# Performance work log

Hardware: AMD Instinct MI355X
Metric: run time of the kernel (lower is better)

## Reference

```python
import jax, jax.numpy as jnp
import numpy as np

N, E, H, DK = 50000, 800000, 8, 32


def setup_inputs() -> dict:
    key = jax.random.key(0)
    ks = jax.random.split(key, 5)
    q = jax.random.normal(ks[0], (N, H, DK), dtype=jnp.float32)
    k = jax.random.normal(ks[1], (N, H, DK), dtype=jnp.float32)
    v = jax.random.normal(ks[2], (N, H, DK), dtype=jnp.float32)
    src = jax.random.randint(ks[3], (E,), 0, N)
    dst = jax.random.randint(ks[4], (E,), 0, N)
    return {"q": q, "k": k, "v": v, "src": src, "dst": dst}


def reference(q, k, v, src, dst):
    # src_dot_dst('k','q','score'): per-edge, per-head dot product  [E, H]
    score = jnp.sum(k[src] * q[dst], axis=-1)
    # scaled_exp('score', sqrt(d_k)): exp(clamp(score/sqrt(d_k), -5, 5))
    inv_scale = 1.0 / jnp.sqrt(jnp.asarray(q.shape[-1], q.dtype))
    score = jnp.exp(jnp.clip(score * inv_scale, -5.0, 5.0))
    n = q.shape[0]
    # send_and_recv(src_mul_edge('v','score'), sum) -> wv[dst] += v[src]*score
    wv = jax.ops.segment_sum(v[src] * score[..., None], dst, num_segments=n)
    # send_and_recv(copy_edge('score'), sum) -> z[dst] += score
    z = jax.ops.segment_sum(score, dst, num_segments=n)
    return wv, z
```

## Files before the change

kernel.cpp:

```cpp
#include <hip/hip_runtime.h>
#include <math.h>

#define HEADS 8
#define DKDIM 32
#define REC   (HEADS * DKDIM)

__device__ __forceinline__ unsigned short f2bf_rne(float f) {
    unsigned int u = __float_as_uint(f);
    unsigned int r = u + 0x7fffu + ((u >> 16) & 1u);
    return (unsigned short)(r >> 16);
}
__device__ __forceinline__ float lo16(unsigned int u) { return __uint_as_float(u << 16); }
__device__ __forceinline__ float hi16(unsigned int u) { return __uint_as_float(u & 0xffff0000u); }

__global__ __launch_bounds__(256) void prep_kernel(
    const float* __restrict__ k, const float* __restrict__ v,
    uint4* __restrict__ kvb, int total_chunks,
    const int* __restrict__ dst, int* __restrict__ hist, int E)
{
    const int stride = gridDim.x * blockDim.x;
    for (int i = blockIdx.x * blockDim.x + threadIdx.x; i < total_chunks; i += stride) {
        const float4 kf = ((const float4*)k)[i];
        const float4 vf = ((const float4*)v)[i];
        uint4 o;
        o.x = (unsigned)f2bf_rne(kf.x) | ((unsigned)f2bf_rne(kf.y) << 16);
        o.y = (unsigned)f2bf_rne(kf.z) | ((unsigned)f2bf_rne(kf.w) << 16);
        o.z = (unsigned)f2bf_rne(vf.x) | ((unsigned)f2bf_rne(vf.y) << 16);
        o.w = (unsigned)f2bf_rne(vf.z) | ((unsigned)f2bf_rne(vf.w) << 16);
        kvb[i] = o;
    }
    for (int i = blockIdx.x * blockDim.x + threadIdx.x; i < E; i += stride) {
        atomicAdd(&hist[dst[i]], 1);
    }
}

__global__ __launch_bounds__(256) void scan_part_kernel(const int* __restrict__ hist,
                                                        int* __restrict__ bsum, int n) {
    const int t = threadIdx.x, lane = t & 63, wid = t >> 6;
    const int i = blockIdx.x * 256 + t;
    int x = (i < n) ? hist[i] : 0;
    #pragma unroll
    for (int off = 1; off < 64; off <<= 1) x += __shfl_xor(x, off, 64);
    __shared__ int ws[4];
    if (lane == 0) ws[wid] = x;
    __syncthreads();
    if (t == 0) bsum[blockIdx.x] = ws[0] + ws[1] + ws[2] + ws[3];
}

__global__ __launch_bounds__(256) void scan_block_kernel(int* __restrict__ bsum, int nb) {
    const int t = threadIdx.x, lane = t & 63, wid = t >> 6;
    int x = (t < nb) ? bsum[t] : 0;
    int inc = x;
    #pragma unroll
    for (int off = 1; off < 64; off <<= 1) {
        int y = __shfl_up(inc, off, 64);
        if (lane >= off) inc += y;
    }
    __shared__ int ws[4];
    if (lane == 63) ws[wid] = inc;
    __syncthreads();
    int base = 0;
    for (int w = 0; w < wid; ++w) base += ws[w];
    if (t < nb) bsum[t] = base + inc - x;
}

__global__ __launch_bounds__(256) void scan_fix_kernel(const int* __restrict__ hist,
                                                       const int* __restrict__ bsum,
                                                       int* __restrict__ rowptr, int n) {
    const int t = threadIdx.x, lane = t & 63, wid = t >> 6;
    const int i = blockIdx.x * 256 + t;
    int x = (i < n) ? hist[i] : 0;
    int inc = x;
    #pragma unroll
    for (int off = 1; off < 64; off <<= 1) {
        int y = __shfl_up(inc, off, 64);
        if (lane >= off) inc += y;
    }
    __shared__ int ws[4];
    if (lane == 63) ws[wid] = inc;
    __syncthreads();
    int base = bsum[blockIdx.x];
    for (int w = 0; w < wid; ++w) base += ws[w];
    if (i < n) rowptr[i] = base + inc - x;
}

__global__ void scatter_kernel(const int* __restrict__ src, const int* __restrict__ dst,
                               int* __restrict__ rowptr,
                               int* __restrict__ sorted_src, int E) {
    int i = blockIdx.x * blockDim.x + threadIdx.x;
    const int stride = gridDim.x * blockDim.x;
    for (; i < E; i += stride) {
        const int pos = atomicAdd(&rowptr[dst[i]], 1);
        sorted_src[pos] = src[i];
    }
}

__global__ __launch_bounds__(256) void node_kernel_bf16(
    const float* __restrict__ q, const uint4* __restrict__ kvb,
    const int* __restrict__ rowptr, const int* __restrict__ hist,
    const int* __restrict__ sorted_src,
    float* __restrict__ wv, float* __restrict__ z, int nodes)
{
    const int lane = threadIdx.x & 63;
    const int node = blockIdx.x * 4 + (threadIdx.x >> 6);
    if (node >= nodes) return;
    const int h = lane >> 3;
    const float inv_scale = 0.17677669529663687f;

    const float4 qf = ((const float4*)(q + (size_t)node * REC))[lane];
    float4 acc = {0.f, 0.f, 0.f, 0.f};
    float zacc = 0.f;

    const int end = rowptr[node];
    const int beg = end - hist[node];
    int i = beg;
    for (; i + 3 < end; i += 4) {
        const int s0 = sorted_src[i];
        const int s1 = sorted_src[i + 1];
        const int s2 = sorted_src[i + 2];
        const int s3 = sorted_src[i + 3];
        const uint4 c0 = kvb[(size_t)s0 * 64 + lane];
        const uint4 c1 = kvb[(size_t)s1 * 64 + lane];
        const uint4 c2 = kvb[(size_t)s2 * 64 + lane];
        const uint4 c3 = kvb[(size_t)s3 * 64 + lane];

        float p0 = lo16(c0.x) * qf.x + hi16(c0.x) * qf.y + lo16(c0.y) * qf.z + hi16(c0.y) * qf.w;
        float p1 = lo16(c1.x) * qf.x + hi16(c1.x) * qf.y + lo16(c1.y) * qf.z + hi16(c1.y) * qf.w;
        float p2 = lo16(c2.x) * qf.x + hi16(c2.x) * qf.y + lo16(c2.y) * qf.z + hi16(c2.y) * qf.w;
        float p3 = lo16(c3.x) * qf.x + hi16(c3.x) * qf.y + lo16(c3.y) * qf.z + hi16(c3.y) * qf.w;
        p0 += __shfl_xor(p0, 4, 8); p1 += __shfl_xor(p1, 4, 8);
        p2 += __shfl_xor(p2, 4, 8); p3 += __shfl_xor(p3, 4, 8);
        p0 += __shfl_xor(p0, 2, 8); p1 += __shfl_xor(p1, 2, 8);
        p2 += __shfl_xor(p2, 2, 8); p3 += __shfl_xor(p3, 2, 8);
        p0 += __shfl_xor(p0, 1, 8); p1 += __shfl_xor(p1, 1, 8);
        p2 += __shfl_xor(p2, 1, 8); p3 += __shfl_xor(p3, 1, 8);
        const float sc0 = __expf(fminf(fmaxf(p0 * inv_scale, -5.0f), 5.0f));
        const float sc1 = __expf(fminf(fmaxf(p1 * inv_scale, -5.0f), 5.0f));
        const float sc2 = __expf(fminf(fmaxf(p2 * inv_scale, -5.0f), 5.0f));
        const float sc3 = __expf(fminf(fmaxf(p3 * inv_scale, -5.0f), 5.0f));

        acc.x += lo16(c0.z) * sc0 + lo16(c1.z) * sc1 + lo16(c2.z) * sc2 + lo16(c3.z) * sc3;
        acc.y += hi16(c0.z) * sc0 + hi16(c1.z) * sc1 + hi16(c2.z) * sc2 + hi16(c3.z) * sc3;
        acc.z += lo16(c0.w) * sc0 + lo16(c1.w) * sc1 + lo16(c2.w) * sc2 + lo16(c3.w) * sc3;
        acc.w += hi16(c0.w) * sc0 + hi16(c1.w) * sc1 + hi16(c2.w) * sc2 + hi16(c3.w) * sc3;
        zacc += (sc0 + sc1) + (sc2 + sc3);
    }
    for (; i < end; ++i) {
        const int s0 = sorted_src[i];
        const uint4 c0 = kvb[(size_t)s0 * 64 + lane];
        float p0 = lo16(c0.x) * qf.x + hi16(c0.x) * qf.y + lo16(c0.y) * qf.z + hi16(c0.y) * qf.w;
        p0 += __shfl_xor(p0, 4, 8);
        p0 += __shfl_xor(p0, 2, 8);
        p0 += __shfl_xor(p0, 1, 8);
        const float sc0 = __expf(fminf(fmaxf(p0 * inv_scale, -5.0f), 5.0f));
        acc.x += lo16(c0.z) * sc0;
        acc.y += hi16(c0.z) * sc0;
        acc.z += lo16(c0.w) * sc0;
        acc.w += hi16(c0.w) * sc0;
        zacc += sc0;
    }
    ((float4*)(wv + (size_t)node * REC))[lane] = acc;
    if ((lane & 7) == 0) z[(size_t)node * HEADS + h] = zacc;
}

__global__ __launch_bounds__(256) void node_kernel_f32(
    const float* __restrict__ q, const float* __restrict__ k,
    const float* __restrict__ v,
    const int* __restrict__ rowptr, const int* __restrict__ hist,
    const int* __restrict__ sorted_src,
    float* __restrict__ wv, float* __restrict__ z, int nodes)
{
    const int lane = threadIdx.x & 63;
    const int node = blockIdx.x * 4 + (threadIdx.x >> 6);
    if (node >= nodes) return;
    const int h = lane >> 3;
    const float inv_scale = 0.17677669529663687f;

    const float4 qf = ((const float4*)(q + (size_t)node * REC))[lane];
    float4 acc = {0.f, 0.f, 0.f, 0.f};
    float zacc = 0.f;

    const int end = rowptr[node];
    const int beg = end - hist[node];
    for (int i = beg; i < end; ++i) {
        const int s = sorted_src[i];
        const float4 kf = ((const float4*)(k + (size_t)s * REC))[lane];
        float p = kf.x * qf.x + kf.y * qf.y + kf.z * qf.z + kf.w * qf.w;
        p += __shfl_xor(p, 4, 8);
        p += __shfl_xor(p, 2, 8);
        p += __shfl_xor(p, 1, 8);
        const float score = __expf(fminf(fmaxf(p * inv_scale, -5.0f), 5.0f));
        const float4 vf = ((const float4*)(v + (size_t)s * REC))[lane];
        acc.x += vf.x * score;
        acc.y += vf.y * score;
        acc.z += vf.z * score;
        acc.w += vf.w * score;
        zacc += score;
    }
    ((float4*)(wv + (size_t)node * REC))[lane] = acc;
    if ((lane & 7) == 0) z[(size_t)node * HEADS + h] = zacc;
}

extern "C" void kernel_launch(void* const* d_in, const int* in_sizes, int n_in,
                              void* d_out, int out_size, void* d_ws, size_t ws_size,
                              hipStream_t stream) {
    const float* q  = (const float*)d_in[0];
    const float* k  = (const float*)d_in[1];
    const float* v  = (const float*)d_in[2];
    const int* src  = (const int*)d_in[3];
    const int* dst  = (const int*)d_in[4];
    const int E     = in_sizes[3];
    const int nodes = in_sizes[0] / REC;

    float* wv = (float*)d_out;
    float* z  = wv + (size_t)nodes * REC;

    const int nb = (nodes + 255) / 256;
    const size_t kv_bytes  = (size_t)nodes * 64 * sizeof(uint4);
    const size_t int_count = (size_t)2 * nodes + nb + (size_t)E;
    const bool use_bf16 = ws_size >= kv_bytes + int_count * sizeof(int);

    char* wsb = (char*)d_ws;
    uint4* kvb = (uint4*)wsb;
    int* ints  = use_bf16 ? (int*)(wsb + kv_bytes) : (int*)wsb;
    int* hist       = ints;
    int* rowptr     = hist + nodes;
    int* bsum       = rowptr + nodes;
    int* sorted_src = bsum + nb;

    hipMemsetAsync(hist, 0, (size_t)nodes * sizeof(int), stream);
    if (use_bf16) {
        prep_kernel<<<2048, 256, 0, stream>>>(k, v, kvb, nodes * 64, dst, hist, E);
    } else {
        prep_kernel<<<2048, 256, 0, stream>>>(k, v, kvb, 0, dst, hist, E);
    }
    scan_part_kernel<<<nb, 256, 0, stream>>>(hist, bsum, nodes);
    scan_block_kernel<<<1, 256, 0, stream>>>(bsum, nb);
    scan_fix_kernel<<<nb, 256, 0, stream>>>(hist, bsum, rowptr, nodes);
    scatter_kernel<<<1024, 256, 0, stream>>>(src, dst, rowptr, sorted_src, E);
    if (use_bf16)
        node_kernel_bf16<<<(nodes + 3) / 4, 256, 0, stream>>>(q, kvb, rowptr, hist,
                                                              sorted_src, wv, z, nodes);
    else
        node_kernel_f32<<<(nodes + 3) / 4, 256, 0, stream>>>(q, k, v, rowptr, hist,
                                                             sorted_src, wv, z, nodes);
}
```

Measured before the change: 240.0 us.

## Move bf16 conversion into scatter kernel, use rowptr neighbors, unroll by two

Moves the k/v bf16 packing out of the histogram kernel and into the scatter kernel, leaving a small standalone hist kernel with its own grid size. The node kernels now take segment bounds from adjacent post-scatter rowptr entries instead of reading hist, and make the node index wave-uniform with readfirstlane. The bf16 edge loop is unrolled by two instead of four, which uses fewer registers but keeps fewer gathers in flight. The intent is to rebalance work across the pre-processing kernels and to cut per-node loads and register pressure in the gather kernel.

```diff
diff --git a/kernel.cpp b/kernel.cpp
--- a/kernel.cpp
+++ b/kernel.cpp
@@ -13,25 +13,12 @@
 __device__ __forceinline__ float lo16(unsigned int u) { return __uint_as_float(u << 16); }
 __device__ __forceinline__ float hi16(unsigned int u) { return __uint_as_float(u & 0xffff0000u); }
 
-__global__ __launch_bounds__(256) void prep_kernel(
-    const float* __restrict__ k, const float* __restrict__ v,
-    uint4* __restrict__ kvb, int total_chunks,
+__global__ __launch_bounds__(256) void hist_kernel(
     const int* __restrict__ dst, int* __restrict__ hist, int E)
 {
+    int i = blockIdx.x * blockDim.x + threadIdx.x;
     const int stride = gridDim.x * blockDim.x;
-    for (int i = blockIdx.x * blockDim.x + threadIdx.x; i < total_chunks; i += stride) {
-        const float4 kf = ((const float4*)k)[i];
-        const float4 vf = ((const float4*)v)[i];
-        uint4 o;
-        o.x = (unsigned)f2bf_rne(kf.x) | ((unsigned)f2bf_rne(kf.y) << 16);
-        o.y = (unsigned)f2bf_rne(kf.z) | ((unsigned)f2bf_rne(kf.w) << 16);
-        o.z = (unsigned)f2bf_rne(vf.x) | ((unsigned)f2bf_rne(vf.y) << 16);
-        o.w = (unsigned)f2bf_rne(vf.z) | ((unsigned)f2bf_rne(vf.w) << 16);
-        kvb[i] = o;
-    }
-    for (int i = blockIdx.x * blockDim.x + threadIdx.x; i < E; i += stride) {
-        atomicAdd(&hist[dst[i]], 1);
-    }
+    for (; i < E; i += stride) atomicAdd(&hist[dst[i]], 1);
 }
 
 __global__ __launch_bounds__(256) void scan_part_kernel(const int* __restrict__ hist,
@@ -84,26 +71,38 @@
     if (i < n) rowptr[i] = base + inc - x;
 }
 
-__global__ void scatter_kernel(const int* __restrict__ src, const int* __restrict__ dst,
-                               int* __restrict__ rowptr,
-                               int* __restrict__ sorted_src, int E) {
-    int i = blockIdx.x * blockDim.x + threadIdx.x;
+__global__ __launch_bounds__(256) void scatter_convert_kernel(
+    const int* __restrict__ src, const int* __restrict__ dst,
+    int* __restrict__ rowptr, int* __restrict__ sorted_src, int E,
+    const float* __restrict__ k, const float* __restrict__ v,
+    uint4* __restrict__ kvb, int total_chunks)
+{
     const int stride = gridDim.x * blockDim.x;
-    for (; i < E; i += stride) {
+    for (int i = blockIdx.x * blockDim.x + threadIdx.x; i < E; i += stride) {
         const int pos = atomicAdd(&rowptr[dst[i]], 1);
         sorted_src[pos] = src[i];
     }
+    for (int i = blockIdx.x * blockDim.x + threadIdx.x; i < total_chunks; i += stride) {
+        const float4 kf = ((const float4*)k)[i];
+        const float4 vf = ((const float4*)v)[i];
+        uint4 o;
+        o.x = (unsigned)f2bf_rne(kf.x) | ((unsigned)f2bf_rne(kf.y) << 16);
+        o.y = (unsigned)f2bf_rne(kf.z) | ((unsigned)f2bf_rne(kf.w) << 16);
+        o.z = (unsigned)f2bf_rne(vf.x) | ((unsigned)f2bf_rne(vf.y) << 16);
+        o.w = (unsigned)f2bf_rne(vf.z) | ((unsigned)f2bf_rne(vf.w) << 16);
+        kvb[i] = o;
+    }
 }
 
 __global__ __launch_bounds__(256) void node_kernel_bf16(
     const float* __restrict__ q, const uint4* __restrict__ kvb,
-    const int* __restrict__ rowptr, const int* __restrict__ hist,
-    const int* __restrict__ sorted_src,
+    const int* __restrict__ rowptr, const int* __restrict__ sorted_src,
     float* __restrict__ wv, float* __restrict__ z, int nodes)
 {
     const int lane = threadIdx.x & 63;
-    const int node = blockIdx.x * 4 + (threadIdx.x >> 6);
+    int node = blockIdx.x * 4 + (threadIdx.x >> 6);
     if (node >= nodes) return;
+    node = __builtin_amdgcn_readfirstlane(node);
     const int h = lane >> 3;
     const float inv_scale = 0.17677669529663687f;
 
@@ -111,44 +110,36 @@
     float4 acc = {0.f, 0.f, 0.f, 0.f};
     float zacc = 0.f;
 
+    const int beg = (node > 0) ? rowptr[node - 1] : 0;
     const int end = rowptr[node];
-    const int beg = end - hist[node];
     int i = beg;
-    for (; i + 3 < end; i += 4) {
+    for (; i + 1 < end; i += 2) {
         const int s0 = sorted_src[i];
         const int s1 = sorted_src[i + 1];
-        const int s2 = sorted_src[i + 2];
-        const int s3 = sorted_src[i + 3];
         const uint4 c0 = kvb[(size_t)s0 * 64 + lane];
         const uint4 c1 = kvb[(size_t)s1 * 64 + lane];
-        const uint4 c2 = kvb[(size_t)s2 * 64 + lane];
-        const uint4 c3 = kvb[(size_t)s3 * 64 + lane];
-
-        float p0 = lo16(c0.x) * qf.x + hi16(c0.x) * qf.y + lo16(c0.y) * qf.z + hi16(c0.y) * qf.w;
-        float p1 = lo16(c1.x) * qf.x + hi16(c1.x) * qf.y + lo16(c1.y) * qf.z + hi16(c1.y) * qf.w;
-        float p2 = lo16(c2.x) * qf.x + hi16(c2.x) * qf.y + lo16(c2.y) * qf.z + hi16(c2.y) * qf.w;
-        float p3 = lo16(c3.x) * qf.x + hi16(c3.x) * qf.y + lo16(c3.y) * qf.z + hi16(c3.y) * qf.w;
+
+        float p0 = lo16(c0.x) * qf.x + hi16(c0.x) * qf.y
+                 + lo16(c0.y) * qf.z + hi16(c0.y) * qf.w;
+        float p1 = lo16(c1.x) * qf.x + hi16(c1.x) * qf.y
+                 + lo16(c1.y) * qf.z + hi16(c1.y) * qf.w;
         p0 += __shfl_xor(p0, 4, 8); p1 += __shfl_xor(p1, 4, 8);
-        p2 += __shfl_xor(p2, 4, 8); p3 += __shfl_xor(p3, 4, 8);
         p0 += __shfl_xor(p0, 2, 8); p1 += __shfl_xor(p1, 2, 8);
-        p2 += __shfl_xor(p2, 2, 8); p3 += __shfl_xor(p3, 2, 8);
         p0 += __shfl_xor(p0, 1, 8); p1 += __shfl_xor(p1, 1, 8);
-        p2 += __shfl_xor(p2, 1, 8); p3 += __shfl_xor(p3, 1, 8);
         const float sc0 = __expf(fminf(fmaxf(p0 * inv_scale, -5.0f), 5.0f));
         const float sc1 = __expf(fminf(fmaxf(p1 * inv_scale, -5.0f), 5.0f));
-        const float sc2 = __expf(fminf(fmaxf(p2 * inv_scale, -5.0f), 5.0f));
-        const float sc3 = __expf(fminf(fmaxf(p3 * inv_scale, -5.0f), 5.0f));
-
-        acc.x += lo16(c0.z) * sc0 + lo16(c1.z) * sc1 + lo16(c2.z) * sc2 + lo16(c3.z) * sc3;
-        acc.y += hi16(c0.z) * sc0 + hi16(c1.z) * sc1 + hi16(c2.z) * sc2 + hi16(c3.z) * sc3;
-        acc.z += lo16(c0.w) * sc0 + lo16(c1.w) * sc1 + lo16(c2.w) * sc2 + lo16(c3.w) * sc3;
-        acc.w += hi16(c0.w) * sc0 + hi16(c1.w) * sc1 + hi16(c2.w) * sc2 + hi16(c3.w) * sc3;
-        zacc += (sc0 + sc1) + (sc2 + sc3);
-    }
-    for (; i < end; ++i) {
+
+        acc.x += lo16(c0.z) * sc0 + lo16(c1.z) * sc1;
+        acc.y += hi16(c0.z) * sc0 + hi16(c1.z) * sc1;
+        acc.z += lo16(c0.w) * sc0 + lo16(c1.w) * sc1;
+        acc.w += hi16(c0.w) * sc0 + hi16(c1.w) * sc1;
+        zacc += sc0 + sc1;
+    }
+    if (i < end) {
         const int s0 = sorted_src[i];
         const uint4 c0 = kvb[(size_t)s0 * 64 + lane];
-        float p0 = lo16(c0.x) * qf.x + hi16(c0.x) * qf.y + lo16(c0.y) * qf.z + hi16(c0.y) * qf.w;
+        float p0 = lo16(c0.x) * qf.x + hi16(c0.x) * qf.y
+                 + lo16(c0.y) * qf.z + hi16(c0.y) * qf.w;
         p0 += __shfl_xor(p0, 4, 8);
         p0 += __shfl_xor(p0, 2, 8);
         p0 += __shfl_xor(p0, 1, 8);
@@ -166,13 +157,13 @@
 __global__ __launch_bounds__(256) void node_kernel_f32(
     const float* __restrict__ q, const float* __restrict__ k,
     const float* __restrict__ v,
-    const int* __restrict__ rowptr, const int* __restrict__ hist,
-    const int* __restrict__ sorted_src,
+    const int* __restrict__ rowptr, const int* __restrict__ sorted_src,
     float* __restrict__ wv, float* __restrict__ z, int nodes)
 {
     const int lane = threadIdx.x & 63;
-    const int node = blockIdx.x * 4 + (threadIdx.x >> 6);
+    int node = blockIdx.x * 4 + (threadIdx.x >> 6);
     if (node >= nodes) return;
+    node = __builtin_amdgcn_readfirstlane(node);
     const int h = lane >> 3;
     const float inv_scale = 0.17677669529663687f;
 
@@ -180,8 +171,8 @@
     float4 acc = {0.f, 0.f, 0.f, 0.f};
     float zacc = 0.f;
 
+    const int beg = (node > 0) ? rowptr[node - 1] : 0;
     const int end = rowptr[node];
-    const int beg = end - hist[node];
     for (int i = beg; i < end; ++i) {
         const int s = sorted_src[i];
         const float4 kf = ((const float4*)(k + (size_t)s * REC))[lane];
@@ -215,9 +206,9 @@
     float* wv = (float*)d_out;
     float* z  = wv + (size_t)nodes * REC;
 
-    const int nb = (nodes + 255) / 256;
+    const int nbp = (nodes + 255) / 256;
     const size_t kv_bytes  = (size_t)nodes * 64 * sizeof(uint4);
-    const size_t int_count = (size_t)2 * nodes + nb + (size_t)E;
+    const size_t int_count = (size_t)2 * nodes + nbp + (size_t)E;
     const bool use_bf16 = ws_size >= kv_bytes + int_count * sizeof(int);
 
     char* wsb = (char*)d_ws;
@@ -226,22 +217,19 @@
     int* hist       = ints;
     int* rowptr     = hist + nodes;
     int* bsum       = rowptr + nodes;
-    int* sorted_src = bsum + nb;
+    int* sorted_src = bsum + nbp;
 
     hipMemsetAsync(hist, 0, (size_t)nodes * sizeof(int), stream);
-    if (use_bf16) {
-        prep_kernel<<<2048, 256, 0, stream>>>(k, v, kvb, nodes * 64, dst, hist, E);
-    } else {
-        prep_kernel<<<2048, 256, 0, stream>>>(k, v, kvb, 0, dst, hist, E);
-    }
-    scan_part_kernel<<<nb, 256, 0, stream>>>(hist, bsum, nodes);
-    scan_block_kernel<<<1, 256, 0, stream>>>(bsum, nb);
-    scan_fix_kernel<<<nb, 256, 0, stream>>>(hist, bsum, rowptr, nodes);
-    scatter_kernel<<<1024, 256, 0, stream>>>(src, dst, rowptr, sorted_src, E);
+    hist_kernel<<<800, 256, 0, stream>>>(dst, hist, E);
+    scan_part_kernel<<<nbp, 256, 0, stream>>>(hist, bsum, nodes);
+    scan_block_kernel<<<1, 256, 0, stream>>>(bsum, nbp);
+    scan_fix_kernel<<<nbp, 256, 0, stream>>>(hist, bsum, rowptr, nodes);
+    scatter_convert_kernel<<<2048, 256, 0, stream>>>(
+        src, dst, rowptr, sorted_src, E, k, v, kvb, use_bf16 ? nodes * 64 : 0);
     if (use_bf16)
-        node_kernel_bf16<<<(nodes + 3) / 4, 256, 0, stream>>>(q, kvb, rowptr, hist,
-                                                              sorted_src, wv, z, nodes);
+        node_kernel_bf16<<<(nodes + 3) / 4, 256, 0, stream>>>(
+            q, kvb, rowptr, sorted_src, wv, z, nodes);
     else
-        node_kernel_f32<<<(nodes + 3) / 4, 256, 0, stream>>>(q, k, v, rowptr, hist,
-                                                             sorted_src, wv, z, nodes);
-}
+        node_kernel_f32<<<(nodes + 3) / 4, 256, 0, stream>>>(
+            q, k, v, rowptr, sorted_src, wv, z, nodes);
+}
```

New measurement: 241.2 us. No clear change (+0.5%).
